# Kernel tuning notes

Measured on AMD Instinct MI355X. Metric: run time of the kernel, lower is better.

Reference implementation:

```python
import jax, jax.numpy as jnp
import numpy as np

N, E = 100000, 1000000          # nodes, edges
IN, OUT = 64, 64                # feature dims
R, B = 16, 8                    # num_rels, num_bases


def setup_inputs() -> dict:
    key = jax.random.key(0)
    k = jax.random.split(key, 6)
    h = jax.random.normal(k[0], (N, IN), jnp.float32)
    weight = jax.random.normal(k[1], (B, IN, OUT), jnp.float32) * 0.05
    w_comp = jax.random.normal(k[2], (R, B), jnp.float32) * 0.3
    src = jax.random.randint(k[3], (E,), 0, N, jnp.int32)
    dst = jax.random.randint(k[4], (E,), 0, N, jnp.int32)
    rel = jax.random.randint(k[5], (E,), 0, R, jnp.int32)
    return {"h": h, "weight": weight, "w_comp": w_comp,
            "src": src, "dst": dst, "rel": rel}


def _rel_weights(weight, w_comp):
    # Faithful replication of the torch basis-combination including its
    # exact (reinterpreting) view calls:
    #   weight.view(in, B, out); matmul(w_comp, .); .view(R, in, out)
    V = weight.reshape(IN, B, OUT)                 # reinterpret, not transpose
    M = jnp.einsum('rb,ibo->iro', w_comp, V)       # [IN, R, OUT]
    return M.reshape(R, IN, OUT)


def reference(h, weight, w_comp, src, dst, rel):
    W = _rel_weights(weight, w_comp)               # [R, IN, OUT]
    # msg_e = h[src_e] @ W[rel_e]; computed without materializing [E,IN,OUT]:
    proj = jnp.einsum('nd,rdf->nrf', h, W)         # [N, R, OUT]
    msg = proj[src, rel]                           # [E, OUT] per-edge gather
    h2 = jax.ops.segment_sum(msg, dst, num_segments=N)  # fn.sum -> 'h2'
    # apply_func: bias is None (falsy); returns activation(old h).
    # Note: original apply_func reads but does not use h2 (tutorial quirk);
    # we return both the updated 'h' and the aggregated 'h2'.
    h_new = jax.nn.relu(h)
    return h_new, h2
```

## Files before the change

kernel.cpp:

```cpp
#include <hip/hip_runtime.h>
#include <hip/hip_bf16.h>

#define NN 100000
#define EE 1000000
#define FDIM 64
#define NREL 16
#define NBASE 8
#define HN (NN * FDIM)
#define H4 (HN / 4)
#define WSZ (NREL * FDIM * FDIM)
#define EGX 128

typedef __attribute__((ext_vector_type(8))) short short8;
typedef __attribute__((ext_vector_type(4))) float f32x4;

static __device__ __forceinline__ ushort f2bf(float f) {
    __hip_bfloat16 b = __float2bfloat16(f);
    return *(ushort*)&b;
}

__global__ void compute_wt_kernel(const float* __restrict__ weight,
                                  const float* __restrict__ w_comp,
                                  ushort* __restrict__ WT, int* __restrict__ counts) {
    int q = blockIdx.x * blockDim.x + threadIdx.x;
    if (blockIdx.x == 0 && threadIdx.x < NREL) counts[threadIdx.x] = 0;
    if (q >= WSZ) return;
    int r = q >> 12;
    int o = (q >> 6) & 63;
    int d = q & 63;
    const float* wc = w_comp + (d & 15) * NBASE;
    const float* wv = weight + (size_t)(4 * r + (d >> 4)) * 512 + o;
    float acc = 0.f;
#pragma unroll
    for (int b = 0; b < NBASE; ++b)
        acc = fmaf(wc[b], wv[b * 64], acc);
    WT[q] = f2bf(acc);
}

__global__ void relu_zero_cvt_kernel(const float4* __restrict__ h4,
                                     float4* __restrict__ out4,
                                     ushort2* __restrict__ hb2) {
    int i = blockIdx.x * blockDim.x + threadIdx.x;
    if (i < H4) {
        float4 v = h4[i];
        ushort2 lo, hi;
        lo.x = f2bf(v.x); lo.y = f2bf(v.y);
        hi.x = f2bf(v.z); hi.y = f2bf(v.w);
        hb2[2 * i] = lo;
        hb2[2 * i + 1] = hi;
        v.x = fmaxf(v.x, 0.f); v.y = fmaxf(v.y, 0.f);
        v.z = fmaxf(v.z, 0.f); v.w = fmaxf(v.w, 0.f);
        out4[i] = v;
        out4[H4 + i] = make_float4(0.f, 0.f, 0.f, 0.f);
    }
}

__global__ void hist_kernel(const int* __restrict__ rel, int* __restrict__ counts) {
    __shared__ int lc[NREL];
    if (threadIdx.x < NREL) lc[threadIdx.x] = 0;
    __syncthreads();
    int stride = gridDim.x * blockDim.x;
    for (int i = blockIdx.x * blockDim.x + threadIdx.x; i < EE; i += stride)
        atomicAdd(&lc[rel[i]], 1);
    __syncthreads();
    if (threadIdx.x < NREL && lc[threadIdx.x] > 0)
        atomicAdd(&counts[threadIdx.x], lc[threadIdx.x]);
}

__global__ void scan_kernel(const int* __restrict__ counts,
                            int* __restrict__ offsets, int* __restrict__ cursors) {
    if (threadIdx.x == 0 && blockIdx.x == 0) {
        int acc = 0;
        for (int r = 0; r < NREL; ++r) { offsets[r] = acc; cursors[r] = acc; acc += counts[r]; }
        offsets[NREL] = acc;
    }
}

__global__ void scatter_kernel(const int* __restrict__ rel, const int* __restrict__ src,
                               const int* __restrict__ dst, int* __restrict__ cursors,
                               int* __restrict__ src_bin, int* __restrict__ dst_bin) {
    __shared__ int lhist[NREL];
    __shared__ int lbase[NREL];
    int i = blockIdx.x * blockDim.x + threadIdx.x;
    if (threadIdx.x < NREL) lhist[threadIdx.x] = 0;
    __syncthreads();
    int r = 0, rank = 0;
    if (i < EE) { r = rel[i]; rank = atomicAdd(&lhist[r], 1); }
    __syncthreads();
    if (threadIdx.x < NREL && lhist[threadIdx.x] > 0)
        lbase[threadIdx.x] = atomicAdd(&cursors[threadIdx.x], lhist[threadIdx.x]);
    __syncthreads();
    if (i < EE) {
        int pos = lbase[r] + rank;
        src_bin[pos] = src[i];
        dst_bin[pos] = dst[i];
    }
}

__global__ __launch_bounds__(256) void edge_mfma_kernel(
    const int* __restrict__ offsets, const int* __restrict__ src_bin,
    const int* __restrict__ dst_bin, const ushort* __restrict__ hb,
    const ushort* __restrict__ WT, float* __restrict__ h2) {
    const int rel  = blockIdx.y;
    const int lane = threadIdx.x & 63;
    const int quad = lane >> 4;
    const int l15  = lane & 15;
    const int start = offsets[rel];
    const int end   = offsets[rel + 1];
    const int cnt   = end - start;
    if (cnt <= 0) return;

    const short8* wt = (const short8*)(WT + rel * 4096);
    short8 Bf[2][4];
#pragma unroll
    for (int t = 0; t < 4; ++t) {
#pragma unroll
        for (int s = 0; s < 2; ++s)
            Bf[s][t] = wt[((t * 16 + l15) << 3) + (s << 2) + quad];
    }

    const int nw   = EGX * 4;
    const int wave = blockIdx.x * 4 + (threadIdx.x >> 6);
    const int nb   = (cnt + 15) >> 4;
    const int per  = (nb + nw - 1) / nw;
    int b0 = wave * per;
    int b1 = b0 + per; if (b1 > nb) b1 = nb;

    const int quad4 = quad * 4;

    for (int b = b0; b < b1; ++b) {
        const int base = start + (b << 4);
        int ei = base + l15; if (ei >= end) ei = end - 1;
        int s0 = src_bin[ei];
        const short8* ar = (const short8*)(hb + (size_t)s0 * FDIM);
        short8 A0 = ar[quad];
        short8 A1 = ar[4 + quad];

        f32x4 acc[4];
#pragma unroll
        for (int t = 0; t < 4; ++t) acc[t] = (f32x4){0.f, 0.f, 0.f, 0.f};
#pragma unroll
        for (int t = 0; t < 4; ++t) {
            acc[t] = __builtin_amdgcn_mfma_f32_16x16x32_bf16(A0, Bf[0][t], acc[t], 0, 0, 0);
            acc[t] = __builtin_amdgcn_mfma_f32_16x16x32_bf16(A1, Bf[1][t], acc[t], 0, 0, 0);
        }

#pragma unroll
        for (int r = 0; r < 4; ++r) {
            int em = base + quad4 + r;
            if (em < end) {
                int dv = dst_bin[em];
                float* p = h2 + (size_t)dv * FDIM + l15;
                unsafeAtomicAdd(p,      acc[0][r]);
                unsafeAtomicAdd(p + 16, acc[1][r]);
                unsafeAtomicAdd(p + 32, acc[2][r]);
                unsafeAtomicAdd(p + 48, acc[3][r]);
            }
        }
    }
}

extern "C" void kernel_launch(void* const* d_in, const int* in_sizes, int n_in,
                              void* d_out, int out_size, void* d_ws, size_t ws_size,
                              hipStream_t stream) {
    const float* h      = (const float*)d_in[0];
    const float* weight = (const float*)d_in[1];
    const float* w_comp = (const float*)d_in[2];
    const int*   src    = (const int*)d_in[3];
    const int*   dst    = (const int*)d_in[4];
    const int*   rel    = (const int*)d_in[5];

    float* out_hnew = (float*)d_out;
    float* out_h2   = out_hnew + HN;

    char* ws = (char*)d_ws;
    ushort* WT      = (ushort*)ws;
    int*    meta    = (int*)(ws + 0x20000);
    int*    counts  = meta;
    int*    offsets = meta + 16;
    int*    cursors = meta + 33;
    int*    src_bin = (int*)(ws + 0x20400);
    int*    dst_bin = (int*)(ws + 0x20400 + 4 * EE);
    ushort* hb      = (ushort*)(ws + 0x20400 + 8 * EE);

    hipLaunchKernelGGL(compute_wt_kernel, dim3(WSZ / 256), dim3(256), 0, stream,
                       weight, w_comp, WT, counts);
    hipLaunchKernelGGL(relu_zero_cvt_kernel, dim3((H4 + 255) / 256), dim3(256), 0, stream,
                       (const float4*)h, (float4*)out_hnew, (ushort2*)hb);
    hipLaunchKernelGGL(hist_kernel, dim3(1024), dim3(256), 0, stream, rel, counts);
    hipLaunchKernelGGL(scan_kernel, dim3(1), dim3(64), 0, stream, counts, offsets, cursors);
    hipLaunchKernelGGL(scatter_kernel, dim3((EE + 255) / 256), dim3(256), 0, stream,
                       rel, src, dst, cursors, src_bin, dst_bin);
    hipLaunchKernelGGL(edge_mfma_kernel, dim3(EGX, NREL), dim3(256), 0, stream,
                       offsets, src_bin, dst_bin, hb, WT, out_h2);
}
```

Before: 374.6 us.

## Precompute per-node projections for all relations and aggregate via dst-sorted CSR

Computes h @ W[r] for every node and every relation with an MFMA GEMM into a bf16 projection table. Edges are then sorted by destination through a counting sort, and each destination's messages are gathered and summed in registers with no float atomics. The new path needs a large workspace for the projection table and falls back to the old relation-binned atomic kernel when the workspace is too small. The trade is extra dense GEMM work over all 16 relations per node plus a 200MB table, in exchange for removing the per-edge atomics.

New measurement: 556.9 us. +48.7%, slower.

```diff
diff --git a/kernel.cpp b/kernel.cpp
--- a/kernel.cpp
+++ b/kernel.cpp
@@ -9,6 +9,8 @@
 #define HN (NN * FDIM)
 #define H4 (HN / 4)
 #define WSZ (NREL * FDIM * FDIM)
+#define NPAD 100032
+#define PCOLS 1024
 #define EGX 128
 
 typedef __attribute__((ext_vector_type(8))) short short8;
@@ -18,44 +20,162 @@
     __hip_bfloat16 b = __float2bfloat16(f);
     return *(ushort*)&b;
 }
-
-__global__ void compute_wt_kernel(const float* __restrict__ weight,
-                                  const float* __restrict__ w_comp,
-                                  ushort* __restrict__ WT, int* __restrict__ counts) {
-    int q = blockIdx.x * blockDim.x + threadIdx.x;
-    if (blockIdx.x == 0 && threadIdx.x < NREL) counts[threadIdx.x] = 0;
-    if (q >= WSZ) return;
-    int r = q >> 12;
-    int o = (q >> 6) & 63;
-    int d = q & 63;
-    const float* wc = w_comp + (d & 15) * NBASE;
-    const float* wv = weight + (size_t)(4 * r + (d >> 4)) * 512 + o;
-    float acc = 0.f;
-#pragma unroll
-    for (int b = 0; b < NBASE; ++b)
-        acc = fmaf(wc[b], wv[b * 64], acc);
-    WT[q] = f2bf(acc);
-}
-
-__global__ void relu_zero_cvt_kernel(const float4* __restrict__ h4,
-                                     float4* __restrict__ out4,
-                                     ushort2* __restrict__ hb2) {
-    int i = blockIdx.x * blockDim.x + threadIdx.x;
-    if (i < H4) {
-        float4 v = h4[i];
+static __device__ __forceinline__ float bf2f(ushort u) {
+    unsigned x = ((unsigned)u) << 16;
+    float f;
+    __builtin_memcpy(&f, &x, 4);
+    return f;
+}
+
+__global__ void prep_kernel(const float4* __restrict__ h4, float4* __restrict__ out4,
+                            ushort2* __restrict__ hb2,
+                            const float* __restrict__ weight,
+                            const float* __restrict__ w_comp, ushort* __restrict__ WT,
+                            int* __restrict__ cnt, int czn,
+                            float4* __restrict__ h2z, int zero_h2) {
+    int gid = blockIdx.x * blockDim.x + threadIdx.x;
+    if (gid < czn) cnt[gid] = 0;
+    if (gid < WSZ) {
+        int r = gid >> 12;
+        int o = (gid >> 6) & 63;
+        int d = gid & 63;
+        const float* wc = w_comp + (d & 15) * NBASE;
+        const float* wv = weight + (size_t)(4 * r + (d >> 4)) * 512 + o;
+        float acc = 0.f;
+#pragma unroll
+        for (int b = 0; b < NBASE; ++b)
+            acc = fmaf(wc[b], wv[b * 64], acc);
+        WT[gid] = f2bf(acc);
+    }
+    if (gid < H4) {
+        float4 v = h4[gid];
         ushort2 lo, hi;
         lo.x = f2bf(v.x); lo.y = f2bf(v.y);
         hi.x = f2bf(v.z); hi.y = f2bf(v.w);
-        hb2[2 * i] = lo;
-        hb2[2 * i + 1] = hi;
+        hb2[2 * gid] = lo;
+        hb2[2 * gid + 1] = hi;
         v.x = fmaxf(v.x, 0.f); v.y = fmaxf(v.y, 0.f);
         v.z = fmaxf(v.z, 0.f); v.w = fmaxf(v.w, 0.f);
-        out4[i] = v;
-        out4[H4 + i] = make_float4(0.f, 0.f, 0.f, 0.f);
-    }
-}
-
-__global__ void hist_kernel(const int* __restrict__ rel, int* __restrict__ counts) {
+        out4[gid] = v;
+        if (zero_h2) h2z[gid] = make_float4(0.f, 0.f, 0.f, 0.f);
+    }
+}
+
+
+__global__ __launch_bounds__(256) void proj_gemm_kernel(
+    const ushort* __restrict__ hb, const ushort* __restrict__ WT,
+    ushort* __restrict__ projb, const int* __restrict__ dst, int* __restrict__ cnt) {
+    const int wv = threadIdx.x >> 6;
+    const int lane = threadIdx.x & 63;
+    const int quad = lane >> 4, l15 = lane & 15;
+    const int row0 = blockIdx.x * 64;
+    const int col0 = blockIdx.y * 256 + wv * 64;
+
+    if (blockIdx.y == 0) {
+        int tid = blockIdx.x * 256 + threadIdx.x;
+        int stride = gridDim.x * 256;
+        for (int i = tid; i < EE; i += stride)
+            atomicAdd(&cnt[dst[i]], 1);
+    }
+
+    short8 Af[4][2];
+#pragma unroll
+    for (int g = 0; g < 4; ++g) {
+        const short8* ar = (const short8*)(hb + (size_t)(row0 + 16 * g + l15) * 64);
+        Af[g][0] = ar[quad];
+        Af[g][1] = ar[4 + quad];
+    }
+    short8 Bf[2][4];
+#pragma unroll
+    for (int t = 0; t < 4; ++t) {
+        const short8* br = (const short8*)(WT + (size_t)(col0 + 16 * t + l15) * 64);
+        Bf[0][t] = br[quad];
+        Bf[1][t] = br[4 + quad];
+    }
+    f32x4 acc[4][4];
+#pragma unroll
+    for (int g = 0; g < 4; ++g)
+#pragma unroll
+        for (int t = 0; t < 4; ++t) acc[g][t] = (f32x4){0.f, 0.f, 0.f, 0.f};
+#pragma unroll
+    for (int g = 0; g < 4; ++g)
+#pragma unroll
+        for (int t = 0; t < 4; ++t) {
+            acc[g][t] = __builtin_amdgcn_mfma_f32_16x16x32_bf16(Af[g][0], Bf[0][t], acc[g][t], 0, 0, 0);
+            acc[g][t] = __builtin_amdgcn_mfma_f32_16x16x32_bf16(Af[g][1], Bf[1][t], acc[g][t], 0, 0, 0);
+        }
+#pragma unroll
+    for (int g = 0; g < 4; ++g) {
+        int rbase = row0 + 16 * g + quad * 4;
+#pragma unroll
+        for (int t = 0; t < 4; ++t) {
+            size_t cb = (size_t)(col0 + 16 * t + l15);
+#pragma unroll
+            for (int r = 0; r < 4; ++r)
+                projb[(size_t)(rbase + r) * PCOLS + cb] = f2bf(acc[g][t][r]);
+        }
+    }
+}
+
+#define SCAN_T 1024
+#define SCAN_C 98
+__global__ __launch_bounds__(1024) void scan_dst_kernel(
+    const int* __restrict__ cnt, int* __restrict__ off, int* __restrict__ cur) {
+    __shared__ int lds[SCAN_T];
+    int t = threadIdx.x;
+    int lo = t * SCAN_C, hi = lo + SCAN_C;
+    if (lo > NN) lo = NN;
+    if (hi > NN) hi = NN;
+    int s = 0;
+    for (int i = lo; i < hi; ++i) s += cnt[i];
+    lds[t] = s;
+    __syncthreads();
+    for (int o = 1; o < SCAN_T; o <<= 1) {
+        int v = (t >= o) ? lds[t - o] : 0;
+        __syncthreads();
+        lds[t] += v;
+        __syncthreads();
+    }
+    int base = (t > 0) ? lds[t - 1] : 0;
+    for (int i = lo; i < hi; ++i) { off[i] = base; cur[i] = base; base += cnt[i]; }
+    if (t == SCAN_T - 1) off[NN] = lds[SCAN_T - 1];
+}
+
+__global__ void scatter_dst_kernel(const int* __restrict__ src, const int* __restrict__ dst,
+                                   const int* __restrict__ rel, int* __restrict__ cur,
+                                   int* __restrict__ pidx) {
+    int i = blockIdx.x * blockDim.x + threadIdx.x;
+    if (i < EE) {
+        int pos = atomicAdd(&cur[dst[i]], 1);
+        pidx[pos] = src[i] * 16 + rel[i];
+    }
+}
+
+__global__ __launch_bounds__(256) void aggregate_kernel(
+    const int* __restrict__ off, const int* __restrict__ pidx,
+    const ushort* __restrict__ projb, float* __restrict__ h2) {
+    int wv = (blockIdx.x * 256 + threadIdx.x) >> 6;
+    int lane = threadIdx.x & 63;
+    int v = __builtin_amdgcn_readfirstlane(wv);
+    if (v >= NN) return;
+    int s = off[v], e = off[v + 1];
+    float acc = 0.f;
+    int i = s;
+    for (; i + 4 <= e; i += 4) {
+        int p0 = pidx[i], p1 = pidx[i + 1], p2 = pidx[i + 2], p3 = pidx[i + 3];
+        float a = bf2f(projb[(size_t)p0 * 64 + lane]);
+        float b = bf2f(projb[(size_t)p1 * 64 + lane]);
+        float c = bf2f(projb[(size_t)p2 * 64 + lane]);
+        float d = bf2f(projb[(size_t)p3 * 64 + lane]);
+        acc += (a + b) + (c + d);
+    }
+    for (; i < e; ++i)
+        acc += bf2f(projb[(size_t)pidx[i] * 64 + lane]);
+    h2[(size_t)v * 64 + lane] = acc;
+}
+
+
+__global__ void hist16_kernel(const int* __restrict__ rel, int* __restrict__ counts) {
     __shared__ int lc[NREL];
     if (threadIdx.x < NREL) lc[threadIdx.x] = 0;
     __syncthreads();
@@ -67,8 +187,8 @@
         atomicAdd(&counts[threadIdx.x], lc[threadIdx.x]);
 }
 
-__global__ void scan_kernel(const int* __restrict__ counts,
-                            int* __restrict__ offsets, int* __restrict__ cursors) {
+__global__ void scan16_kernel(const int* __restrict__ counts,
+                              int* __restrict__ offsets, int* __restrict__ cursors) {
     if (threadIdx.x == 0 && blockIdx.x == 0) {
         int acc = 0;
         for (int r = 0; r < NREL; ++r) { offsets[r] = acc; cursors[r] = acc; acc += counts[r]; }
@@ -76,9 +196,9 @@
     }
 }
 
-__global__ void scatter_kernel(const int* __restrict__ rel, const int* __restrict__ src,
-                               const int* __restrict__ dst, int* __restrict__ cursors,
-                               int* __restrict__ src_bin, int* __restrict__ dst_bin) {
+__global__ void scatter16_kernel(const int* __restrict__ rel, const int* __restrict__ src,
+                                 const int* __restrict__ dst, int* __restrict__ cursors,
+                                 int* __restrict__ src_bin, int* __restrict__ dst_bin) {
     __shared__ int lhist[NREL];
     __shared__ int lbase[NREL];
     int i = blockIdx.x * blockDim.x + threadIdx.x;
@@ -101,13 +221,13 @@
     const int* __restrict__ offsets, const int* __restrict__ src_bin,
     const int* __restrict__ dst_bin, const ushort* __restrict__ hb,
     const ushort* __restrict__ WT, float* __restrict__ h2) {
-    const int rel  = blockIdx.y;
+    const int rel = blockIdx.y;
     const int lane = threadIdx.x & 63;
     const int quad = lane >> 4;
-    const int l15  = lane & 15;
+    const int l15 = lane & 15;
     const int start = offsets[rel];
-    const int end   = offsets[rel + 1];
-    const int cnt   = end - start;
+    const int end = offsets[rel + 1];
+    const int cnt = end - start;
     if (cnt <= 0) return;
 
     const short8* wt = (const short8*)(WT + rel * 4096);
@@ -118,14 +238,12 @@
         for (int s = 0; s < 2; ++s)
             Bf[s][t] = wt[((t * 16 + l15) << 3) + (s << 2) + quad];
     }
-
-    const int nw   = EGX * 4;
+    const int nw = EGX * 4;
     const int wave = blockIdx.x * 4 + (threadIdx.x >> 6);
-    const int nb   = (cnt + 15) >> 4;
-    const int per  = (nb + nw - 1) / nw;
+    const int nb = (cnt + 15) >> 4;
+    const int per = (nb + nw - 1) / nw;
     int b0 = wave * per;
     int b1 = b0 + per; if (b1 > nb) b1 = nb;
-
     const int quad4 = quad * 4;
 
     for (int b = b0; b < b1; ++b) {
@@ -135,7 +253,6 @@
         const short8* ar = (const short8*)(hb + (size_t)s0 * FDIM);
         short8 A0 = ar[quad];
         short8 A1 = ar[4 + quad];
-
         f32x4 acc[4];
 #pragma unroll
         for (int t = 0; t < 4; ++t) acc[t] = (f32x4){0.f, 0.f, 0.f, 0.f};
@@ -144,7 +261,6 @@
             acc[t] = __builtin_amdgcn_mfma_f32_16x16x32_bf16(A0, Bf[0][t], acc[t], 0, 0, 0);
             acc[t] = __builtin_amdgcn_mfma_f32_16x16x32_bf16(A1, Bf[1][t], acc[t], 0, 0, 0);
         }
-
 #pragma unroll
         for (int r = 0; r < 4; ++r) {
             int em = base + quad4 + r;
@@ -174,23 +290,54 @@
     float* out_h2   = out_hnew + HN;
 
     char* ws = (char*)d_ws;
-    ushort* WT      = (ushort*)ws;
-    int*    meta    = (int*)(ws + 0x20000);
-    int*    counts  = meta;
-    int*    offsets = meta + 16;
-    int*    cursors = meta + 33;
-    int*    src_bin = (int*)(ws + 0x20400);
-    int*    dst_bin = (int*)(ws + 0x20400 + 4 * EE);
-    ushort* hb      = (ushort*)(ws + 0x20400 + 8 * EE);
-
-    hipLaunchKernelGGL(compute_wt_kernel, dim3(WSZ / 256), dim3(256), 0, stream,
-                       weight, w_comp, WT, counts);
-    hipLaunchKernelGGL(relu_zero_cvt_kernel, dim3((H4 + 255) / 256), dim3(256), 0, stream,
-                       (const float4*)h, (float4*)out_hnew, (ushort2*)hb);
-    hipLaunchKernelGGL(hist_kernel, dim3(1024), dim3(256), 0, stream, rel, counts);
-    hipLaunchKernelGGL(scan_kernel, dim3(1), dim3(64), 0, stream, counts, offsets, cursors);
-    hipLaunchKernelGGL(scatter_kernel, dim3((EE + 255) / 256), dim3(256), 0, stream,
-                       rel, src, dst, cursors, src_bin, dst_bin);
-    hipLaunchKernelGGL(edge_mfma_kernel, dim3(EGX, NREL), dim3(256), 0, stream,
-                       offsets, src_bin, dst_bin, hb, WT, out_h2);
-}
+
+    size_t o_cnt  = 131072;
+    size_t o_off  = o_cnt + 400000;
+    size_t o_cur  = o_off + 400016;
+    size_t o_pidx = o_cur + 400000;
+    size_t o_hb   = o_pidx + 4000000;
+    size_t o_proj = o_hb + (size_t)NPAD * 128;
+    size_t need   = o_proj + (size_t)NPAD * 2048;
+
+    if (ws_size >= need) {
+        ushort* WT    = (ushort*)ws;
+        int*    cnt   = (int*)(ws + o_cnt);
+        int*    off   = (int*)(ws + o_off);
+        int*    cur   = (int*)(ws + o_cur);
+        int*    pidx  = (int*)(ws + o_pidx);
+        ushort* hb    = (ushort*)(ws + o_hb);
+        ushort* projb = (ushort*)(ws + o_proj);
+
+        hipLaunchKernelGGL(prep_kernel, dim3((H4 + 255) / 256), dim3(256), 0, stream,
+                           (const float4*)h, (float4*)out_hnew, (ushort2*)hb,
+                           weight, w_comp, WT, cnt, NN, (float4*)out_h2, 0);
+        hipLaunchKernelGGL(proj_gemm_kernel, dim3(NPAD / 64, 4), dim3(256), 0, stream,
+                           hb, WT, projb, dst, cnt);
+        hipLaunchKernelGGL(scan_dst_kernel, dim3(1), dim3(SCAN_T), 0, stream,
+                           cnt, off, cur);
+        hipLaunchKernelGGL(scatter_dst_kernel, dim3((EE + 255) / 256), dim3(256), 0, stream,
+                           src, dst, rel, cur, pidx);
+        hipLaunchKernelGGL(aggregate_kernel, dim3(NN / 4), dim3(256), 0, stream,
+                           off, pidx, projb, out_h2);
+    } else {
+        ushort* WT      = (ushort*)ws;
+        int*    meta    = (int*)(ws + 0x20000);
+        int*    counts  = meta;
+        int*    offsets = meta + 16;
+        int*    cursors = meta + 33;
+        int*    src_bin = (int*)(ws + 0x20400);
+        int*    dst_bin = (int*)(ws + 0x20400 + 4 * EE);
+        ushort* hb      = (ushort*)(ws + 0x20400 + 8 * EE);
+
+        hipLaunchKernelGGL(prep_kernel, dim3((H4 + 255) / 256), dim3(256), 0, stream,
+                           (const float4*)h, (float4*)out_hnew, (ushort2*)hb,
+                           weight, w_comp, WT, counts, 16, (float4*)out_h2, 1);
+        hipLaunchKernelGGL(hist16_kernel, dim3(1024), dim3(256), 0, stream, rel, counts);
+        hipLaunchKernelGGL(scan16_kernel, dim3(1), dim3(64), 0, stream,
+                           counts, offsets, cursors);
+        hipLaunchKernelGGL(scatter16_kernel, dim3((EE + 255) / 256), dim3(256), 0, stream,
+                           rel, src, dst, cursors, src_bin, dst_bin);
+        hipLaunchKernelGGL(edge_mfma_kernel, dim3(EGX, NREL), dim3(256), 0, stream,
+                           offsets, src_bin, dst_bin, hb, WT, out_h2);
+    }
+}
```
